# Performance work log

Hardware: AMD Instinct MI355X
Metric: run time of the kernel (lower is better)

## Reference

```python
import jax, jax.numpy as jnp
import numpy as np


def setup_inputs() -> dict:
    key = jax.random.key(0)
    ks = jax.random.split(key, 8)
    B, C, N = 4, 256, 4096
    C4 = C // 4
    x = jax.random.normal(ks[0], (B, C, N), dtype=jnp.float32)
    # conv1x1 weights == channel-mixing matrices [out_ch, in_ch]
    Wq = jax.random.normal(ks[1], (C4, C), dtype=jnp.float32) * (1.0 / np.sqrt(C))
    bq = jax.random.normal(ks[2], (C4,), dtype=jnp.float32) * 0.02
    Wk = jax.random.normal(ks[3], (C4, C), dtype=jnp.float32) * (1.0 / np.sqrt(C))
    bk = jax.random.normal(ks[4], (C4,), dtype=jnp.float32) * 0.02
    Wv = jax.random.normal(ks[5], (C, C), dtype=jnp.float32) * (1.0 / np.sqrt(C))
    bv = jax.random.normal(ks[6], (C,), dtype=jnp.float32) * 0.02
    # nn.Parameter(torch.zeros(1)) -> but use nonzero so grads flow through attn path
    gamma = jax.random.normal(ks[7], (1,), dtype=jnp.float32) * 0.1
    return {"x": x, "Wq": Wq, "bq": bq, "Wk": Wk, "bk": bk,
            "Wv": Wv, "bv": bv, "gamma": gamma}


def reference(x, Wq, bq, Wk, bk, Wv, bv, gamma):
    # x: [B, C, N]; conv1x1 == matmul over channel dim
    q = jnp.einsum('oc,bcn->bon', Wq, x) + bq[None, :, None]   # [B, C/4, N]
    k = jnp.einsum('oc,bcn->bon', Wk, x) + bk[None, :, None]   # [B, C/4, N]
    v = jnp.einsum('oc,bcn->bon', Wv, x) + bv[None, :, None]   # [B, C,   N]
    # energy[b, i, j] = <q[:, i], k[:, j]>  (unscaled)
    energy = jnp.einsum('bdi,bdj->bij', q, k)                  # [B, N, N]
    attn = jax.nn.softmax(energy, axis=-1)                     # softmax over j
    # out[b, c, i] = sum_j v[b, c, j] * attn[b, i, j]
    out = jnp.einsum('bcj,bij->bci', v, attn)                  # [B, C, N]
    return gamma[0] * out + x
```

## Files before the change

kernel.cpp:

```cpp
#include <hip/hip_runtime.h>

#define NPTS 4096
#define CDIM 256
#define C4DIM 64

typedef __bf16 bf16x8 __attribute__((ext_vector_type(8)));
typedef float  f32x4  __attribute__((ext_vector_type(4)));

__device__ __forceinline__ void async_cp16(const void* g, void* l) {
    __builtin_amdgcn_global_load_lds(
        (const __attribute__((address_space(1))) void*)g,
        (__attribute__((address_space(3))) void*)l, 16, 0, 0);
}

__global__ __launch_bounds__(256) void wprep_kernel(
    const float* __restrict__ Wq, const float* __restrict__ Wk,
    const float* __restrict__ Wv, __bf16* __restrict__ wsz)
{
    int idx = blockIdx.x * 256 + threadIdx.x;
    int row = idx >> 6;
    int l   = idx & 63;
    const float* src;
    if (row < 64)       src = Wq + (size_t)row * CDIM;
    else if (row < 128) src = Wk + (size_t)(row - 64) * CDIM;
    else                src = Wv + (size_t)(row - 128) * CDIM;
    float4 f = *(const float4*)&src[l * 4];
    int g  = l >> 1;
    int gp = g ^ (row & 7);
    union { __bf16 h[4]; uint2 u; } pk;
    pk.h[0] = (__bf16)f.x; pk.h[1] = (__bf16)f.y;
    pk.h[2] = (__bf16)f.z; pk.h[3] = (__bf16)f.w;
    *(uint2*)&wsz[(size_t)row * CDIM + gp * 8 + (l & 1) * 4] = pk.u;
}

__global__ __launch_bounds__(256, 2) void proj_kernel(
    const float* __restrict__ x,
    const float* __restrict__ bq, const float* __restrict__ bk,
    const float* __restrict__ bv, const __bf16* __restrict__ wsz,
    __bf16* __restrict__ qT, __bf16* __restrict__ kT, __bf16* __restrict__ vo)
{
    __shared__ __align__(16) unsigned char sm[65536];
    auto Xs = (float (*)[33])sm;

    const int t    = threadIdx.x;
    const int w    = t >> 6;
    const int lane = t & 63;
    const int quad = lane >> 4;
    const int l16  = lane & 15;
    const int nq   = w >> 1;
    const int th   = w & 1;

    const int n0 = blockIdx.x * 32;
    const int b  = blockIdx.y;

    #pragma unroll
    for (int s = 0; s < 8; s++) {
        int lin = t + 256 * s;
        int c = lin >> 3, n4 = (lin & 7) * 4;
        *(float4*)&Xs[c][n4] =
            *(const float4*)&x[((size_t)b * CDIM + c) * NPTS + n0 + n4];
    }
    __syncthreads();

    bf16x8 af[8];
    #pragma unroll
    for (int kc = 0; kc < 8; kc++) {
        union { __bf16 h8[8]; bf16x8 v; } pk;
        #pragma unroll
        for (int u = 0; u < 8; u++)
            pk.h8[u] = (__bf16)Xs[kc * 32 + quad * 8 + u][16 * nq + l16];
        af[kc] = pk.v;
    }
    __syncthreads();

    const int lhalf = lane >> 5;
    const int rlow  = (2 * w + lhalf) & 7;
    const int slane = ((lane & 31) ^ rlow) * 8;

    #pragma unroll
    for (int s = 0; s < 8; s++)
        async_cp16(wsz + (size_t)(8 * s + 2 * w + lhalf) * CDIM + slane,
                   sm + (s * 4 + w) * 1024);

    f32x4 acc[6][2];
    #pragma unroll
    for (int ot = 0; ot < 6; ot++) {
        acc[ot][0] = (f32x4)(0.f);
        acc[ot][1] = (f32x4)(0.f);
    }

    #pragma unroll
    for (int ot = 0; ot < 6; ot++) {
        __syncthreads();
        if (ot < 5) {
            #pragma unroll
            for (int s = 0; s < 8; s++)
                async_cp16(wsz + (size_t)((ot + 1) * 64 + 8 * s + 2 * w + lhalf) * CDIM + slane,
                           sm + ((ot + 1) & 1) * 32768 + (s * 4 + w) * 1024);
        }
        const unsigned char* Wp = sm + (ot & 1) * 32768;
        #pragma unroll
        for (int kc = 0; kc < 8; kc++) {
            bf16x8 bw[2];
            #pragma unroll
            for (int tcl = 0; tcl < 2; tcl++)
                bw[tcl] = *(const bf16x8*)(Wp + (16 * (2 * th + tcl) + l16) * 512
                                              + (((kc * 4 + quad) ^ (l16 & 7)) << 4));
            #pragma unroll
            for (int tcl = 0; tcl < 2; tcl++)
                acc[ot][tcl] = __builtin_amdgcn_mfma_f32_16x16x32_bf16(
                    af[kc], bw[tcl], acc[ot][tcl], 0, 0, 0);
        }
    }

    {
        auto OT = (float (*)[68])sm;
        #pragma unroll
        for (int ot = 0; ot < 2; ot++) {
            __syncthreads();
            const float* bias = ot ? bk : bq;
            #pragma unroll
            for (int tcl = 0; tcl < 2; tcl++) {
                float bs = bias[16 * (2 * th + tcl) + l16];
                #pragma unroll
                for (int r4 = 0; r4 < 4; r4++)
                    OT[16 * nq + 4 * quad + r4][16 * (2 * th + tcl) + l16] =
                        acc[ot][tcl][r4] + bs;
            }
            __syncthreads();
            __bf16* outp = (ot == 0 ? qT : kT) + (size_t)b * NPTS * C4DIM;
            int n = t >> 3, op = (t & 7) * 8;
            f32x4 o0 = *(const f32x4*)&OT[n][op];
            f32x4 o1 = *(const f32x4*)&OT[n][op + 4];
            union { __bf16 h[8]; uint4 u; } pk;
            #pragma unroll
            for (int u2 = 0; u2 < 4; u2++) {
                pk.h[u2]     = (__bf16)o0[u2];
                pk.h[u2 + 4] = (__bf16)o1[u2];
            }
            *(uint4*)&outp[(size_t)(n0 + n) * C4DIM + op] = pk.u;
        }
    }
    {
        auto OTv = (float (*)[36])sm;
        #pragma unroll
        for (int ot = 2; ot < 6; ot++) {
            __syncthreads();
            #pragma unroll
            for (int tcl = 0; tcl < 2; tcl++) {
                float bs = bv[(ot - 2) * 64 + 16 * (2 * th + tcl) + l16];
                f32x4 v4 = acc[ot][tcl];
                v4[0] += bs; v4[1] += bs; v4[2] += bs; v4[3] += bs;
                *(f32x4*)&OTv[16 * (2 * th + tcl) + l16][16 * nq + 4 * quad] = v4;
            }
            __syncthreads();
            int cl = t >> 2, np = (t & 3) * 8;
            int ch = (ot - 2) * 64 + cl;
            f32x4 o0 = *(const f32x4*)&OTv[cl][np];
            f32x4 o1 = *(const f32x4*)&OTv[cl][np + 4];
            union { __bf16 h[8]; uint4 u; } pk;
            #pragma unroll
            for (int u2 = 0; u2 < 4; u2++) {
                pk.h[u2]     = (__bf16)o0[u2];
                pk.h[u2 + 4] = (__bf16)o1[u2];
            }
            *(uint4*)&vo[((size_t)b * CDIM + ch) * NPTS + n0 + np] = pk.u;
        }
    }
}

__global__ __launch_bounds__(256, 2) void attn_kernel(
    const __bf16* __restrict__ qT, const __bf16* __restrict__ kT,
    const __bf16* __restrict__ vin, const float* __restrict__ xin,
    const float* __restrict__ gptr, float* __restrict__ out)
{
    __shared__ __align__(16) unsigned char sm[58368];
    unsigned char* Kb = sm;
    unsigned char* Vb = sm + 16384;
    auto Ps  = (__bf16 (*)[72])(sm + 49152);
    auto OTa = (float (*)[68])sm;
    float* Lp = (float*)(sm + 34816);

    const int t    = threadIdx.x;
    const int w    = t >> 6;
    const int lane = t & 63;
    const int quad = lane >> 4;
    const int l16  = lane & 15;
    const int r    = w >> 1;
    const int jh   = w & 1;

    const int b  = blockIdx.z;
    const int i0 = blockIdx.x * 64;
    const int c0 = blockIdx.y * 128;

    const __bf16* qb = qT  + (size_t)b * NPTS * C4DIM;
    const __bf16* kb = kT  + (size_t)b * NPTS * C4DIM;
    const __bf16* vb = vin + (size_t)b * CDIM * NPTS;

    const int swz = (lane & 7) ^ ((lane >> 3) & 7);
    int koff[2], voff[4];
    #pragma unroll
    for (int s = 0; s < 2; s++) {
        int row = (2 * w + s) * 8 + (lane >> 3);
        koff[s] = row * 128 + swz * 16;
    }
    #pragma unroll
    for (int s = 0; s < 4; s++) {
        int row = (4 * w + s) * 8 + (lane >> 3);
        voff[s] = (c0 + row) * (NPTS * 2) + swz * 16;
    }

    bf16x8 aq[2][2];
    #pragma unroll
    for (int rt = 0; rt < 2; rt++)
        #pragma unroll
        for (int kc = 0; kc < 2; kc++)
            aq[rt][kc] = *(const bf16x8*)&qb[(size_t)(i0 + 32 * r + 16 * rt + l16) * C4DIM
                                             + kc * 32 + quad * 8];

    bf16x8 vone;
    #pragma unroll
    for (int u = 0; u < 8; u++) vone[u] = (__bf16)1.0f;

    f32x4 O[2][8], lacc[2];
    #pragma unroll
    for (int rt = 0; rt < 2; rt++) {
        lacc[rt] = (f32x4)(0.f);
        #pragma unroll
        for (int tc = 0; tc < 8; tc++) O[rt][tc] = (f32x4)(0.f);
    }

    {
        const char* kbase = (const char*)kb;
        const char* vbase = (const char*)vb;
        #pragma unroll
        for (int s = 0; s < 2; s++) async_cp16(kbase + koff[s], Kb + (2 * w + s) * 1024);
        #pragma unroll
        for (int s = 0; s < 4; s++) async_cp16(vbase + voff[s], Vb + (4 * w + s) * 1024);
    }

    int p = 0;
    for (int j0 = 0; j0 < NPTS; j0 += 64, p ^= 1) {
        __syncthreads();

        if (j0 + 64 < NPTS) {
            const char* kbase = (const char*)kb + (size_t)(j0 + 64) * (C4DIM * 2);
            const char* vbase = (const char*)vb + (size_t)(j0 + 64) * 2;
            unsigned char* Kd = Kb + (p ^ 1) * 8192;
            unsigned char* Vd = Vb + (p ^ 1) * 16384;
            #pragma unroll
            for (int s = 0; s < 2; s++) async_cp16(kbase + koff[s], Kd + (2 * w + s) * 1024);
            #pragma unroll
            for (int s = 0; s < 4; s++) async_cp16(vbase + voff[s], Vd + (4 * w + s) * 1024);
        }

        const unsigned char* K = Kb + p * 8192;
        const unsigned char* V = Vb + p * 16384;

        f32x4 S[2][2];
        #pragma unroll
        for (int rt = 0; rt < 2; rt++)
            #pragma unroll
            for (int ct = 0; ct < 2; ct++) S[rt][ct] = (f32x4)(0.f);
        #pragma unroll
        for (int kc = 0; kc < 2; kc++) {
            bf16x8 bk2[2];
            #pragma unroll
            for (int ct = 0; ct < 2; ct++) {
                int row = 32 * jh + 16 * ct + l16;
                int slot = (kc * 4 + quad) ^ (l16 & 7);
                bk2[ct] = *(const bf16x8*)(K + row * 128 + slot * 16);
            }
            #pragma unroll
            for (int rt = 0; rt < 2; rt++)
                #pragma unroll
                for (int ct = 0; ct < 2; ct++)
                    S[rt][ct] = __builtin_amdgcn_mfma_f32_16x16x32_bf16(
                        aq[rt][kc], bk2[ct], S[rt][ct], 0, 0, 0);
        }

        #pragma unroll
        for (int rt = 0; rt < 2; rt++)
            #pragma unroll
            for (int ct = 0; ct < 2; ct++)
                #pragma unroll
                for (int r4 = 0; r4 < 4; r4++)
                    Ps[32 * r + 16 * rt + 4 * quad + r4][32 * jh + 16 * ct + l16] =
                        (__bf16)__builtin_amdgcn_exp2f(
                            __builtin_fmaf(S[rt][ct][r4], 1.44269504088896340736f,
                                           -46.16624130844683f));

        bf16x8 ap[2];
        #pragma unroll
        for (int rt = 0; rt < 2; rt++)
            ap[rt] = *(const bf16x8*)((const char*)&Ps[32 * r + 16 * rt + l16][0]
                                      + jh * 64 + quad * 16);
        __builtin_amdgcn_s_setprio(1);
        #pragma unroll
        for (int tc = 0; tc < 8; tc++) {
            int row = 16 * tc + l16;
            int slot = (jh * 4 + quad) ^ (l16 & 7);
            bf16x8 bv2 = *(const bf16x8*)(V + row * 128 + slot * 16);
            #pragma unroll
            for (int rt = 0; rt < 2; rt++)
                O[rt][tc] = __builtin_amdgcn_mfma_f32_16x16x32_bf16(
                    ap[rt], bv2, O[rt][tc], 0, 0, 0);
        }
        #pragma unroll
        for (int rt = 0; rt < 2; rt++)
            lacc[rt] = __builtin_amdgcn_mfma_f32_16x16x32_bf16(ap[rt], vone, lacc[rt], 0, 0, 0);
        __builtin_amdgcn_s_setprio(0);
    }

    __syncthreads();
    const float g = gptr[0];

    if (jh == 1) {
        float* dst = (float*)(sm + (size_t)(r * 64 + lane) * 272);
        #pragma unroll
        for (int rt = 0; rt < 2; rt++)
            #pragma unroll
            for (int tc = 0; tc < 8; tc++)
                *(f32x4*)(dst + (rt * 8 + tc) * 4) = O[rt][tc];
        if (l16 == 0) {
            #pragma unroll
            for (int rt = 0; rt < 2; rt++)
                #pragma unroll
                for (int r4 = 0; r4 < 4; r4++)
                    Lp[32 * r + 16 * rt + 4 * quad + r4] = lacc[rt][r4];
        }
    }
    __syncthreads();

    float inv[2][4];
    if (jh == 0) {
        const float* src = (const float*)(sm + (size_t)(r * 64 + lane) * 272);
        #pragma unroll
        for (int rt = 0; rt < 2; rt++)
            #pragma unroll
            for (int tc = 0; tc < 8; tc++)
                O[rt][tc] += *(const f32x4*)(src + (rt * 8 + tc) * 4);
        #pragma unroll
        for (int rt = 0; rt < 2; rt++)
            #pragma unroll
            for (int r4 = 0; r4 < 4; r4++) {
                float ls = lacc[rt][r4] + Lp[32 * r + 16 * rt + 4 * quad + r4];
                inv[rt][r4] = g / ls;
            }
    }
    __syncthreads();

    if (jh == 0) {
        #pragma unroll
        for (int rt = 0; rt < 2; rt++)
            #pragma unroll
            for (int tc = 0; tc < 8; tc++) {
                int c = 16 * tc + l16;
                float4 f;
                f.x = O[rt][tc][0] * inv[rt][0];
                f.y = O[rt][tc][1] * inv[rt][1];
                f.z = O[rt][tc][2] * inv[rt][2];
                f.w = O[rt][tc][3] * inv[rt][3];
                *(float4*)&OTa[c][32 * r + 16 * rt + 4 * quad] = f;
            }
    }
    __syncthreads();

    const float* xb = xin + (size_t)b * CDIM * NPTS;
    float*       ob = out + (size_t)b * CDIM * NPTS;
    #pragma unroll
    for (int s = 0; s < 8; s++) {
        int lin = t + 256 * s;
        int c = lin >> 4, col = (lin & 15) * 4;
        size_t gi = (size_t)(c0 + c) * NPTS + i0 + col;
        float4 ov = *(const float4*)&OTa[c][col];
        float4 xv = *(const float4*)&xb[gi];
        float4 rr;
        rr.x = ov.x + xv.x; rr.y = ov.y + xv.y;
        rr.z = ov.z + xv.z; rr.w = ov.w + xv.w;
        *(float4*)&ob[gi] = rr;
    }
}

extern "C" void kernel_launch(void* const* d_in, const int* in_sizes, int n_in,
                              void* d_out, int out_size, void* d_ws, size_t ws_size,
                              hipStream_t stream) {
    const float* x     = (const float*)d_in[0];
    const float* Wq    = (const float*)d_in[1];
    const float* bq    = (const float*)d_in[2];
    const float* Wk    = (const float*)d_in[3];
    const float* bk    = (const float*)d_in[4];
    const float* Wv    = (const float*)d_in[5];
    const float* bv    = (const float*)d_in[6];
    const float* gamma = (const float*)d_in[7];

    const int B = 4;
    __bf16* qT  = (__bf16*)d_ws;
    __bf16* kT  = qT + (size_t)B * NPTS * C4DIM;
    __bf16* v   = kT + (size_t)B * NPTS * C4DIM;
    __bf16* wsz = v  + (size_t)B * CDIM * NPTS;

    wprep_kernel<<<96, 256, 0, stream>>>(Wq, Wk, Wv, wsz);

    proj_kernel<<<dim3(NPTS/32, B), 256, 0, stream>>>(
        x, bq, bk, bv, wsz, qT, kT, v);

    attn_kernel<<<dim3(NPTS/64, CDIM/128, B), 256, 0, stream>>>(
        qT, kT, v, x, gamma, (float*)d_out);
}
```

Baseline: 163.4 us.

## Keep softmax probabilities in registers by transposing QK MFMA operands

The QK^T product now uses K as the A operand and Q as the B operand, so each lane's score accumulator already matches the A-operand layout for the PV product. P stays in registers as bf16 and feeds 16x16x16 MFMAs directly, which removes the LDS write and read of P and shrinks shared memory from 58 KB to 48 KB. In exchange, PV needs twice as many smaller MFMA instructions and 8-byte V reads from LDS instead of 16-byte reads.

```diff
diff --git a/kernel.cpp b/kernel.cpp
--- a/kernel.cpp
+++ b/kernel.cpp
@@ -5,7 +5,10 @@
 #define C4DIM 64
 
 typedef __bf16 bf16x8 __attribute__((ext_vector_type(8)));
+typedef short  s16x4  __attribute__((ext_vector_type(4)));
 typedef float  f32x4  __attribute__((ext_vector_type(4)));
+
+#define MFMA16(a, b, c) __builtin_amdgcn_mfma_f32_16x16x16bf16_1k((a), (b), (c), 0, 0, 0)
 
 __device__ __forceinline__ void async_cp16(const void* g, void* l) {
     __builtin_amdgcn_global_load_lds(
@@ -174,12 +177,9 @@
     const __bf16* __restrict__ vin, const float* __restrict__ xin,
     const float* __restrict__ gptr, float* __restrict__ out)
 {
-    __shared__ __align__(16) unsigned char sm[58368];
+    __shared__ __align__(16) unsigned char sm[49152];
     unsigned char* Kb = sm;
     unsigned char* Vb = sm + 16384;
-    auto Ps  = (__bf16 (*)[72])(sm + 49152);
-    auto OTa = (float (*)[68])sm;
-    float* Lp = (float*)(sm + 34816);
 
     const int t    = threadIdx.x;
     const int w    = t >> 6;
@@ -218,9 +218,13 @@
             aq[rt][kc] = *(const bf16x8*)&qb[(size_t)(i0 + 32 * r + 16 * rt + l16) * C4DIM
                                              + kc * 32 + quad * 8];
 
-    bf16x8 vone;
-    #pragma unroll
-    for (int u = 0; u < 8; u++) vone[u] = (__bf16)1.0f;
+    s16x4 vone4;
+    {
+        union { __bf16 h[4]; s16x4 s; } o;
+        #pragma unroll
+        for (int u = 0; u < 4; u++) o.h[u] = (__bf16)1.0f;
+        vone4 = o.s;
+    }
 
     f32x4 O[2][8], lacc[2];
     #pragma unroll
@@ -259,61 +263,59 @@
 
         f32x4 S[2][2];
         #pragma unroll
-        for (int rt = 0; rt < 2; rt++)
-            #pragma unroll
-            for (int ct = 0; ct < 2; ct++) S[rt][ct] = (f32x4)(0.f);
+        for (int jt = 0; jt < 2; jt++)
+            #pragma unroll
+            for (int it = 0; it < 2; it++) S[jt][it] = (f32x4)(0.f);
         #pragma unroll
         for (int kc = 0; kc < 2; kc++) {
-            bf16x8 bk2[2];
-            #pragma unroll
-            for (int ct = 0; ct < 2; ct++) {
-                int row = 32 * jh + 16 * ct + l16;
+            bf16x8 ka[2];
+            #pragma unroll
+            for (int jt = 0; jt < 2; jt++) {
+                int row = 32 * jh + 16 * jt + l16;
                 int slot = (kc * 4 + quad) ^ (l16 & 7);
-                bk2[ct] = *(const bf16x8*)(K + row * 128 + slot * 16);
-            }
-            #pragma unroll
-            for (int rt = 0; rt < 2; rt++)
+                ka[jt] = *(const bf16x8*)(K + row * 128 + slot * 16);
+            }
+            #pragma unroll
+            for (int jt = 0; jt < 2; jt++)
                 #pragma unroll
-                for (int ct = 0; ct < 2; ct++)
-                    S[rt][ct] = __builtin_amdgcn_mfma_f32_16x16x32_bf16(
-                        aq[rt][kc], bk2[ct], S[rt][ct], 0, 0, 0);
-        }
-
-        #pragma unroll
-        for (int rt = 0; rt < 2; rt++)
-            #pragma unroll
-            for (int ct = 0; ct < 2; ct++)
+                for (int it = 0; it < 2; it++)
+                    S[jt][it] = __builtin_amdgcn_mfma_f32_16x16x32_bf16(
+                        ka[jt], aq[it][kc], S[jt][it], 0, 0, 0);
+        }
+
+        union { __bf16 h[4]; s16x4 s; } pa[2][2];
+        #pragma unroll
+        for (int it = 0; it < 2; it++)
+            #pragma unroll
+            for (int jt = 0; jt < 2; jt++)
                 #pragma unroll
                 for (int r4 = 0; r4 < 4; r4++)
-                    Ps[32 * r + 16 * rt + 4 * quad + r4][32 * jh + 16 * ct + l16] =
-                        (__bf16)__builtin_amdgcn_exp2f(
-                            __builtin_fmaf(S[rt][ct][r4], 1.44269504088896340736f,
-                                           -46.16624130844683f));
-
-        bf16x8 ap[2];
-        #pragma unroll
-        for (int rt = 0; rt < 2; rt++)
-            ap[rt] = *(const bf16x8*)((const char*)&Ps[32 * r + 16 * rt + l16][0]
-                                      + jh * 64 + quad * 16);
+                    pa[it][jt].h[r4] = (__bf16)__builtin_amdgcn_exp2f(
+                        __builtin_fmaf(S[jt][it][r4], 1.44269504088896340736f,
+                                       -46.16624130844683f));
+
         __builtin_amdgcn_s_setprio(1);
         #pragma unroll
-        for (int tc = 0; tc < 8; tc++) {
-            int row = 16 * tc + l16;
-            int slot = (jh * 4 + quad) ^ (l16 & 7);
-            bf16x8 bv2 = *(const bf16x8*)(V + row * 128 + slot * 16);
-            #pragma unroll
-            for (int rt = 0; rt < 2; rt++)
-                O[rt][tc] = __builtin_amdgcn_mfma_f32_16x16x32_bf16(
-                    ap[rt], bv2, O[rt][tc], 0, 0, 0);
-        }
-        #pragma unroll
-        for (int rt = 0; rt < 2; rt++)
-            lacc[rt] = __builtin_amdgcn_mfma_f32_16x16x32_bf16(ap[rt], vone, lacc[rt], 0, 0, 0);
+        for (int jt = 0; jt < 2; jt++) {
+            #pragma unroll
+            for (int tc = 0; tc < 8; tc++) {
+                int row = 16 * tc + l16;
+                int g = (4 * jh + 2 * jt + (quad >> 1)) ^ (l16 & 7);
+                s16x4 vv = *(const s16x4*)(V + row * 128 + g * 16 + (quad & 1) * 8);
+                #pragma unroll
+                for (int it = 0; it < 2; it++)
+                    O[it][tc] = MFMA16(pa[it][jt].s, vv, O[it][tc]);
+            }
+            #pragma unroll
+            for (int it = 0; it < 2; it++)
+                lacc[it] = MFMA16(pa[it][jt].s, vone4, lacc[it]);
+        }
         __builtin_amdgcn_s_setprio(0);
     }
 
     __syncthreads();
     const float g = gptr[0];
+    float* Lp = (float*)(sm + 34816);
 
     if (jh == 1) {
         float* dst = (float*)(sm + (size_t)(r * 64 + lane) * 272);
@@ -350,6 +352,7 @@
     }
     __syncthreads();
 
+    auto OTa = (float (*)[68])sm;
     if (jh == 0) {
         #pragma unroll
         for (int rt = 0; rt < 2; rt++)
```

Result: no change. 162.6 us (-0.5%).
